# Kernel optimization log

Measured on AMD Instinct MI355X. Metric: run time of the kernel, lower is better.

The kernel has to match this reference:

```python
import jax, jax.numpy as jnp
import numpy as np
import math

D_MODEL = 512
N_HEADS = 8
D_K = D_MODEL // N_HEADS
N_SAMPLES = 16
BETA = 1.0
SCALE = 1.0 / math.sqrt(D_K)
PROPOSAL_TEMP = 0.5


def setup_inputs() -> dict:
    key = jax.random.key(0)
    ks = jax.random.split(key, 9)
    B, S = 2, 512
    x = jax.random.normal(ks[0], (B, S, D_MODEL), dtype=jnp.float32)
    init = lambda k: jax.random.normal(k, (D_MODEL, D_MODEL), dtype=jnp.float32) * 0.02
    return {
        "x": x,
        "Wq": init(ks[1]), "bq": jnp.zeros((D_MODEL,), jnp.float32),
        "Wk": init(ks[2]), "bk": jnp.zeros((D_MODEL,), jnp.float32),
        "Wv": init(ks[3]), "bv": jnp.zeros((D_MODEL,), jnp.float32),
        "Wo": init(ks[4]), "bo": jnp.zeros((D_MODEL,), jnp.float32),
    }


def _importance_sampled_weights(scores):
    # scores: [B,H,S,S]. Replicates the per-row Python loop, fully vectorized.
    B, H, Sq, Sk = scores.shape
    target = jax.nn.softmax(scores * BETA, axis=-1)            # [B,H,Sq,Sk]
    # optimal proposal: 0.5*target + 0.5*uniform
    prop = PROPOSAL_TEMP * target + (1.0 - PROPOSAL_TEMP) / Sk
    R = B * H * Sq
    tf = target.reshape(R, Sk)
    pf = prop.reshape(R, Sk)
    # tsu_backend.sample_binary_layer(log(p/(1-p))) == Bernoulli(p) sampling
    s = jax.random.bernoulli(jax.random.key(42), pf[:, None, :], (R, N_SAMPLES, Sk))
    # importance weight = prod(target[sel]) / (prod(prop[sel]) * prod(1-prop[~sel]))
    pt = jnp.prod(jnp.where(s, tf[:, None, :], 1.0), axis=-1)                 # [R,N]
    pp = jnp.prod(jnp.where(s, pf[:, None, :], 1.0 - pf[:, None, :]), axis=-1)
    valid = (s.sum(-1) > 0) & (pp > 0)
    w = jnp.where(valid, pt / jnp.maximum(pp, 1e-38), 0.0)
    ws = w.sum(-1, keepdims=True)
    w = jnp.where(ws > 0, w / jnp.maximum(ws, 1e-38), 1.0 / N_SAMPLES)        # [R,N]
    wa = jnp.einsum('rn,rnk->rk', w, s.astype(jnp.float32))                   # [R,Sk]
    was = wa.sum(-1, keepdims=True)
    wa = jnp.where(was > 0, wa / jnp.maximum(was, 1e-38), 1.0 / Sk)
    return wa.reshape(B, H, Sq, Sk)


def reference(x, Wq, bq, Wk, bk, Wv, bv, Wo, bo):
    B, S, Dm = x.shape
    proj = lambda W, b: (x @ W + b).reshape(B, S, N_HEADS, D_K).transpose(0, 2, 1, 3)
    Q = proj(Wq, bq)  # [B,H,S,dk]
    K = proj(Wk, bk)
    V = proj(Wv, bv)
    scores = jnp.einsum('bhqd,bhkd->bhqk', Q, K) * SCALE
    # torch builds weights via torch.tensor(...) which detaches => constant w.r.t. params
    attn = jax.lax.stop_gradient(_importance_sampled_weights(scores))
    out = jnp.einsum('bhqk,bhkd->bhqd', attn, V)
    out = out.transpose(0, 2, 1, 3).reshape(B, S, Dm)
    return out @ Wo + bo
```

## Files before the change

kernel.cpp:

```cpp
#include <hip/hip_runtime.h>
#include <cstdint>
#include <cstddef>


#define ROTL(x, r) __builtin_rotateleft32((x), (r))

#define QR8(s)                                                                \
  x0[0]+=x1[0];x0[1]+=x1[1];x0[2]+=x1[2];x0[3]+=x1[3];                        \
  x0[4]+=x1[4];x0[5]+=x1[5];x0[6]+=x1[6];x0[7]+=x1[7];                        \
  x1[0]=ROTL(x1[0],s);x1[1]=ROTL(x1[1],s);x1[2]=ROTL(x1[2],s);                \
  x1[3]=ROTL(x1[3],s);x1[4]=ROTL(x1[4],s);x1[5]=ROTL(x1[5],s);                \
  x1[6]=ROTL(x1[6],s);x1[7]=ROTL(x1[7],s);                                    \
  x1[0]^=x0[0];x1[1]^=x0[1];x1[2]^=x0[2];x1[3]^=x0[3];                        \
  x1[4]^=x0[4];x1[5]^=x0[5];x1[6]^=x0[6];x1[7]^=x0[7];
#define INJ8(X, Y)                                                            \
  x0[0]+=(X);x0[1]+=(X);x0[2]+=(X);x0[3]+=(X);                                \
  x0[4]+=(X);x0[5]+=(X);x0[6]+=(X);x0[7]+=(X);                                \
  x1[0]+=(Y);x1[1]+=(Y);x1[2]+=(Y);x1[3]+=(Y);                                \
  x1[4]+=(Y);x1[5]+=(Y);x1[6]+=(Y);x1[7]+=(Y);
#define INJ8Y(Y)                                                              \
  x1[0]+=(Y);x1[1]+=(Y);x1[2]+=(Y);x1[3]+=(Y);                                \
  x1[4]+=(Y);x1[5]+=(Y);x1[6]+=(Y);x1[7]+=(Y);

#define WAVE_FENCE() asm volatile("s_waitcnt lgkmcnt(0)" ::: "memory")

__global__ __launch_bounds__(256)
void qkv_gemm(const float* __restrict__ x,
              const float* __restrict__ Wq, const float* __restrict__ bq,
              const float* __restrict__ Wk, const float* __restrict__ bk,
              const float* __restrict__ Wv, const float* __restrict__ bv,
              const float* __restrict__ bo, float* __restrict__ outp,
              float* __restrict__ Qw, float* __restrict__ KTw,
              float* __restrict__ Vw) {
  const int tid = threadIdx.x;
  if (blockIdx.z == 3) {
    const int blk = blockIdx.y * 32 + blockIdx.x;
    const size_t base4 = (size_t)blk * 512 + tid;
    const float4* bo4 = (const float4*)bo;
    float4* out4 = (float4*)outp;
    out4[base4] = bo4[base4 & 127];
    out4[base4 + 256] = bo4[(base4 + 256) & 127];
    return;
  }
  const float* W; const float* bias;
  if (blockIdx.z == 0)      { W = Wq; bias = bq; }
  else if (blockIdx.z == 1) { W = Wk; bias = bk; }
  else                      { W = Wv; bias = bv; }

  __shared__ __align__(16) float smem[32 * 34 + 32 * 64];
  float (*At)[34] = (float(*)[34])smem;
  float (*Bs)[64] = (float(*)[64])(smem + 32 * 34);
  float (*T2)[34] = (float(*)[34])smem;

  const int tx = tid & 15, ty = tid >> 4;
  const int row0 = blockIdx.x * 32, col0 = blockIdx.y * 64;
  float acc[2][4] = {};

  const int ar = tid >> 3;
  const int kc = (tid & 7) << 2;
  const int br0 = tid >> 4,         bc0 = (tid & 15) << 2;
  const int br1 = (tid + 256) >> 4, bc1 = ((tid + 256) & 15) << 2;

  float4 aR, bR0, bR1;
  aR  = *(const float4*)&x[(size_t)(row0 + ar) * 512 + kc];
  bR0 = *(const float4*)&W[(size_t)br0 * 512 + col0 + bc0];
  bR1 = *(const float4*)&W[(size_t)br1 * 512 + col0 + bc1];

  for (int kk = 0; kk < 512; kk += 32) {
    At[kc + 0][ar] = aR.x; At[kc + 1][ar] = aR.y;
    At[kc + 2][ar] = aR.z; At[kc + 3][ar] = aR.w;
    *(float4*)&Bs[br0][bc0] = bR0;
    *(float4*)&Bs[br1][bc1] = bR1;
    __syncthreads();
    if (kk < 480) {
      const int kn = kk + 32;
      aR  = *(const float4*)&x[(size_t)(row0 + ar) * 512 + kn + kc];
      bR0 = *(const float4*)&W[(size_t)(kn + br0) * 512 + col0 + bc0];
      bR1 = *(const float4*)&W[(size_t)(kn + br1) * 512 + col0 + bc1];
    }
#pragma unroll
    for (int p = 0; p < 32; ++p) {
      const float2 a2 = *(const float2*)&At[p][ty << 1];
      const float4 b4 = *(const float4*)&Bs[p][tx << 2];
      acc[0][0] = fmaf(a2.x, b4.x, acc[0][0]); acc[0][1] = fmaf(a2.x, b4.y, acc[0][1]);
      acc[0][2] = fmaf(a2.x, b4.z, acc[0][2]); acc[0][3] = fmaf(a2.x, b4.w, acc[0][3]);
      acc[1][0] = fmaf(a2.y, b4.x, acc[1][0]); acc[1][1] = fmaf(a2.y, b4.y, acc[1][1]);
      acc[1][2] = fmaf(a2.y, b4.z, acc[1][2]); acc[1][3] = fmaf(a2.y, b4.w, acc[1][3]);
    }
    __syncthreads();
  }

  const int h = blockIdx.y;
  if (blockIdx.z == 0 || blockIdx.z == 2) {
    float* dst = (blockIdx.z == 0) ? Qw : Vw;
#pragma unroll
    for (int i = 0; i < 2; ++i) {
      const int row = row0 + (ty << 1) + i;
      const int b = row >> 9, s = row & 511;
#pragma unroll
      for (int j = 0; j < 4; ++j) {
        const int col = col0 + (tx << 2) + j;
        const int d = col & 63;
        dst[(((size_t)(b * 8 + h) * 512 + s) * 64) + d] = acc[i][j] + bias[col];
      }
    }
  } else {
#pragma unroll
    for (int i = 0; i < 2; ++i) {
#pragma unroll
      for (int j = 0; j < 4; ++j) {
        const int col = col0 + (tx << 2) + j;
        T2[(tx << 2) + j][(ty << 1) + i] = acc[i][j] + bias[col];
      }
    }
    __syncthreads();
    const int b = row0 >> 9;
    const int s0 = row0 & 511;
#pragma unroll
    for (int i2 = 0; i2 < 2; ++i2) {
      const int idx = tid + (i2 << 8);
      const int c = idx >> 3, seg = idx & 7;
      float* dst = KTw + (((size_t)(b * 8 + h) * 64 + c) << 9) + s0 + (seg << 2);
      *(float4*)dst = *(const float4*)&T2[c][seg << 2];
    }
  }
}

__global__ __launch_bounds__(256)
void fused_sample(const float* __restrict__ Q, const float* __restrict__ KT,
                  const float* __restrict__ V, const float* __restrict__ Wo,
                  float* __restrict__ outp) {
  const int tid = threadIdx.x;
  const int w = tid >> 6, l = tid & 63;
  const int blk = blockIdx.x;
  const int swz = ((blk & 7) << 8) | (blk >> 3);
  const int r = (swz << 2) + w;
  const int bh = r >> 9, q = r & 511;
  const int b = r >> 12, h = (r >> 9) & 7;

  __shared__ __align__(16) float    qs[4][64];
  __shared__ __align__(16) float    tfs[4][512];
  __shared__ __align__(16) uint32_t thru[4][512];

  float* tf = tfs[w];
  uint32_t* thr = thru[w];
  uint4* thr4 = (uint4*)thr;
  float* wa = (float*)thr;

  qs[w][l] = Q[((size_t)bh * 512 + q) * 64 + l];
  WAVE_FENCE();

  float s0 = 0.f, s1 = 0.f, s2 = 0.f, s3 = 0.f;
  float s4 = 0.f, s5 = 0.f, s6 = 0.f, s7 = 0.f;
  {
    const float* Kp = KT + (size_t)bh * 64 * 512 + (l << 2);
#pragma unroll 4
    for (int d4 = 0; d4 < 16; ++d4) {
      const float4 qv = *(const float4*)&qs[w][d4 << 2];
#pragma unroll
      for (int c = 0; c < 4; ++c) {
        const float qd = (c == 0) ? qv.x : (c == 1) ? qv.y : (c == 2) ? qv.z : qv.w;
        const size_t off = (size_t)(d4 * 4 + c) * 512;
        const float4 ka = *(const float4*)&Kp[off];
        const float4 kb = *(const float4*)&Kp[off + 256];
        s0 = fmaf(qd, ka.x, s0); s1 = fmaf(qd, ka.y, s1);
        s2 = fmaf(qd, ka.z, s2); s3 = fmaf(qd, ka.w, s3);
        s4 = fmaf(qd, kb.x, s4); s5 = fmaf(qd, kb.y, s5);
        s6 = fmaf(qd, kb.z, s6); s7 = fmaf(qd, kb.w, s7);
      }
    }
    s0 *= 0.125f; s1 *= 0.125f; s2 *= 0.125f; s3 *= 0.125f;
    s4 *= 0.125f; s5 *= 0.125f; s6 *= 0.125f; s7 *= 0.125f;
  }

  float mx = fmaxf(fmaxf(fmaxf(s0, s1), fmaxf(s2, s3)),
                   fmaxf(fmaxf(s4, s5), fmaxf(s6, s7)));
#pragma unroll
  for (int m = 1; m < 64; m <<= 1) mx = fmaxf(mx, __shfl_xor(mx, m));
  const float e0 = expf(s0 - mx), e1 = expf(s1 - mx);
  const float e2 = expf(s2 - mx), e3 = expf(s3 - mx);
  const float e4 = expf(s4 - mx), e5 = expf(s5 - mx);
  const float e6 = expf(s6 - mx), e7 = expf(s7 - mx);
  float tot = ((e0 + e1) + (e2 + e3)) + ((e4 + e5) + (e6 + e7));
#pragma unroll
  for (int m = 1; m < 64; m <<= 1) tot += __shfl_xor(tot, m);
  const float t0 = e0 / tot, t1 = e1 / tot, t2 = e2 / tot, t3 = e3 / tot;
  const float t4 = e4 / tot, t5 = e5 / tot, t6 = e6 / tot, t7 = e7 / tot;
  const float p0 = fmaf(0.5f, t0, 0.0009765625f);
  const float p1 = fmaf(0.5f, t1, 0.0009765625f);
  const float p2 = fmaf(0.5f, t2, 0.0009765625f);
  const float p3 = fmaf(0.5f, t3, 0.0009765625f);
  const float p4 = fmaf(0.5f, t4, 0.0009765625f);
  const float p5 = fmaf(0.5f, t5, 0.0009765625f);
  const float p6 = fmaf(0.5f, t6, 0.0009765625f);
  const float p7 = fmaf(0.5f, t7, 0.0009765625f);
  {
    *(float4*)&tf[l << 2]         = make_float4(t0, t1, t2, t3);
    *(float4*)&tf[256 + (l << 2)] = make_float4(t4, t5, t6, t7);
    uint4 ta, tb;
    ta.x = ((uint32_t)ceilf(p0 * 8388608.0f)) << 9;
    ta.y = ((uint32_t)ceilf(p1 * 8388608.0f)) << 9;
    ta.z = ((uint32_t)ceilf(p2 * 8388608.0f)) << 9;
    ta.w = ((uint32_t)ceilf(p3 * 8388608.0f)) << 9;
    tb.x = ((uint32_t)ceilf(p4 * 8388608.0f)) << 9;
    tb.y = ((uint32_t)ceilf(p5 * 8388608.0f)) << 9;
    tb.z = ((uint32_t)ceilf(p6 * 8388608.0f)) << 9;
    tb.w = ((uint32_t)ceilf(p7 * 8388608.0f)) << 9;
    thr4[((l & 31) << 2) + (l >> 5)]     = ta;
    thr4[((l & 31) << 2) + (l >> 5) + 2] = tb;
  }
  float ql = (((1.f - p0) * (1.f - p1)) * ((1.f - p2) * (1.f - p3))) *
             (((1.f - p4) * (1.f - p5)) * ((1.f - p6) * (1.f - p7)));
#pragma unroll
  for (int m = 1; m < 64; m <<= 1) ql *= __shfl_xor(ql, m);
  const float Qrow = ql;
  WAVE_FENCE();

  const int n = l >> 2, gl = l & 3;
  const uint32_t cbase =
      (uint32_t)r * 8192u + (uint32_t)n * 512u + (uint32_t)(gl << 7) + 42u;
  unsigned long long lo = 0ull, hi = 0ull;
  for (int u = 0; u < 16; ++u) {
    uint32_t x0[8], x1[8];
    const uint32_t cb = cbase + (uint32_t)(u << 3);
#pragma unroll
    for (int i = 0; i < 8; ++i) {
      const uint32_t c = cb + (uint32_t)i;
      x0[i] = c;
      x1[i] = ROTL(c, 13) ^ c;
    }
    QR8(15) QR8(26) QR8(6)
    INJ8(42u, 0x1BD11BF1u)
    QR8(17) QR8(29) QR8(16) QR8(24)
    INJ8(0x1BD11BF0u, 2u)
    QR8(13) QR8(15) QR8(26) QR8(6)
    INJ8Y(45u)
    QR8(17) QR8(29) QR8(16) QR8(24)
    INJ8(42u, 0x1BD11BF4u)
    QR8(13) QR8(15) QR8(26) QR8(6)
    INJ8(0x1BD11BF0u, 5u)
    const uint4 pA = thr4[(u << 3) + gl];
    const uint4 pB = thr4[(u << 3) + 4 + gl];
    uint32_t byte = 0u;
    byte |= (uint32_t)((x0[0] ^ x1[0]) < pA.x) << 0;
    byte |= (uint32_t)((x0[1] ^ x1[1]) < pA.y) << 1;
    byte |= (uint32_t)((x0[2] ^ x1[2]) < pA.z) << 2;
    byte |= (uint32_t)((x0[3] ^ x1[3]) < pA.w) << 3;
    byte |= (uint32_t)((x0[4] ^ x1[4]) < pB.x) << 4;
    byte |= (uint32_t)((x0[5] ^ x1[5]) < pB.y) << 5;
    byte |= (uint32_t)((x0[6] ^ x1[6]) < pB.z) << 6;
    byte |= (uint32_t)((x0[7] ^ x1[7]) < pB.w) << 7;
    const int sh = (u & 7) << 3;
    if (u < 8) lo |= (unsigned long long)byte << sh;
    else       hi |= (unsigned long long)byte << sh;
  }

  float ptl = 1.f, ratl = 1.f;
  int cl = __popcll(lo) + __popcll(hi);
  {
    unsigned long long bb = lo;
    while (bb) {
      const int j = __builtin_ctzll(bb);
      bb &= bb - 1ull;
      const float tv = tf[(gl << 7) + j];
      const float p = fmaf(0.5f, tv, 0.0009765625f);
      ptl *= tv;
      ratl *= p / (1.f - p);
    }
    bb = hi;
    while (bb) {
      const int j = __builtin_ctzll(bb);
      bb &= bb - 1ull;
      const float tv = tf[(gl << 7) + 64 + j];
      const float p = fmaf(0.5f, tv, 0.0009765625f);
      ptl *= tv;
      ratl *= p / (1.f - p);
    }
  }
#pragma unroll
  for (int m = 1; m < 4; m <<= 1) {
    ptl *= __shfl_xor(ptl, m);
    ratl *= __shfl_xor(ratl, m);
    cl += __shfl_xor(cl, m);
  }
  const float pp = Qrow * ratl;
  const float wl = (cl > 0 && pp > 0.f) ? (ptl / fmaxf(pp, 1e-38f)) : 0.f;
  float wsum = (gl == 0) ? wl : 0.f;
#pragma unroll
  for (int m = 1; m < 64; m <<= 1) wsum += __shfl_xor(wsum, m);
  const float wn = (wsum > 0.f) ? (wl / fmaxf(wsum, 1e-38f)) : 0.0625f;

  WAVE_FENCE();
  *(float4*)&wa[l << 2]         = make_float4(0.f, 0.f, 0.f, 0.f);
  *(float4*)&wa[256 + (l << 2)] = make_float4(0.f, 0.f, 0.f, 0.f);
  WAVE_FENCE();
  {
    unsigned long long bb = lo;
    while (bb) {
      const int j = __builtin_ctzll(bb);
      bb &= bb - 1ull;
      atomicAdd(&wa[(gl << 7) + j], wn);
    }
    bb = hi;
    while (bb) {
      const int j = __builtin_ctzll(bb);
      bb &= bb - 1ull;
      atomicAdd(&wa[(gl << 7) + 64 + j], wn);
    }
  }
  WAVE_FENCE();

  float sp = 0.f;
#pragma unroll
  for (int c = 0; c < 8; ++c) sp += wa[(c << 6) + l];
#pragma unroll
  for (int m = 1; m < 64; m <<= 1) sp += __shfl_xor(sp, m);
  const float was = sp;

  const float* Vb = V + ((size_t)(b * 8 + h) * 512) * 64;
  float o = 0.f;
  if (was > 0.f) {
    const float inv = 1.f / fmaxf(was, 1e-38f);
#pragma unroll 1
    for (int c = 0; c < 8; ++c) {
      const float v = wa[(c << 6) + l];
      unsigned long long mask = __ballot(v > 0.f);
      while (mask) {
        const int j = __builtin_ctzll(mask);
        mask &= mask - 1ull;
        const int k = (c << 6) + j;
        const float wv = wa[k];
        o = fmaf(wv * inv, Vb[(size_t)k * 64 + l], o);
      }
    }
  } else {
    for (int k = 0; k < 512; ++k) o += Vb[(size_t)k * 64 + l];
    o *= 0.001953125f;
  }

  {
    const float* Wh = Wo + ((size_t)h * 64) * 512 + l;
    float a0 = 0.f, a1 = 0.f, a2 = 0.f, a3 = 0.f;
    float a4 = 0.f, a5 = 0.f, a6 = 0.f, a7 = 0.f;
#pragma unroll 4
    for (int dd = 0; dd < 64; ++dd) {
      const float ov = __shfl(o, dd);
      const float* wrow = Wh + (size_t)dd * 512;
      a0 = fmaf(ov, wrow[0],   a0);
      a1 = fmaf(ov, wrow[64],  a1);
      a2 = fmaf(ov, wrow[128], a2);
      a3 = fmaf(ov, wrow[192], a3);
      a4 = fmaf(ov, wrow[256], a4);
      a5 = fmaf(ov, wrow[320], a5);
      a6 = fmaf(ov, wrow[384], a6);
      a7 = fmaf(ov, wrow[448], a7);
    }
    float* orow = outp + ((size_t)(b * 512 + q)) * 512 + l;
    atomicAdd(&orow[0],   a0);
    atomicAdd(&orow[64],  a1);
    atomicAdd(&orow[128], a2);
    atomicAdd(&orow[192], a3);
    atomicAdd(&orow[256], a4);
    atomicAdd(&orow[320], a5);
    atomicAdd(&orow[384], a6);
    atomicAdd(&orow[448], a7);
  }
}

extern "C" void kernel_launch(void* const* d_in, const int* in_sizes, int n_in,
                              void* d_out, int out_size, void* d_ws,
                              size_t ws_size, hipStream_t stream) {
  const float* x  = (const float*)d_in[0];
  const float* Wq = (const float*)d_in[1];
  const float* bq = (const float*)d_in[2];
  const float* Wk = (const float*)d_in[3];
  const float* bk = (const float*)d_in[4];
  const float* Wv = (const float*)d_in[5];
  const float* bv = (const float*)d_in[6];
  const float* Wo = (const float*)d_in[7];
  const float* bo = (const float*)d_in[8];
  float* out = (float*)d_out;

  float* ws = (float*)d_ws;
  float* Qw = ws;
  float* KT = ws + 524288;
  float* Vw = ws + 1048576;

  dim3 gq(32, 8, 4);
  qkv_gemm<<<gq, 256, 0, stream>>>(x, Wq, bq, Wk, bk, Wv, bv, bo, out,
                                   Qw, KT, Vw);
  fused_sample<<<2048, 256, 0, stream>>>(Qw, KT, Vw, Wo, out);
}
```

Baseline: 283.4 us.

## Share K and Wo loads across the block's four query rows and double-buffer the projection GEMM

The projection GEMM now double-buffers its shared-memory tiles, so each k-step needs one barrier instead of two and the next tile's stores follow the compute. In the sampling kernel, the QK^T scores are computed cooperatively: each thread reads K once and produces scores for all four query rows of the block, instead of each wave reading K separately. The Wo output projection likewise loads each Wo element once per block for four rows, using a shared transposed buffer of the head outputs. This cuts global and L2 traffic for K and Wo by about four times, at the cost of extra block-wide barriers and more shared memory.

Result: faster. 274.9 us (-3.0%).

```diff
diff --git a/kernel.cpp b/kernel.cpp
--- a/kernel.cpp
+++ b/kernel.cpp
@@ -47,10 +47,12 @@
   else if (blockIdx.z == 1) { W = Wk; bias = bk; }
   else                      { W = Wv; bias = bv; }
 
-  __shared__ __align__(16) float smem[32 * 34 + 32 * 64];
-  float (*At)[34] = (float(*)[34])smem;
-  float (*Bs)[64] = (float(*)[64])(smem + 32 * 34);
-  float (*T2)[34] = (float(*)[34])smem;
+  __shared__ __align__(16) float smem[2 * (32 * 34 + 32 * 64)];
+  float (*At0)[34] = (float(*)[34])smem;
+  float (*Bs0)[64] = (float(*)[64])(smem + 32 * 34);
+  float (*At1)[34] = (float(*)[34])(smem + 3136);
+  float (*Bs1)[64] = (float(*)[64])(smem + 3136 + 32 * 34);
+  float (*T2)[34]  = (float(*)[34])smem;
 
   const int tx = tid & 15, ty = tid >> 4;
   const int row0 = blockIdx.x * 32, col0 = blockIdx.y * 64;
@@ -66,12 +68,16 @@
   bR0 = *(const float4*)&W[(size_t)br0 * 512 + col0 + bc0];
   bR1 = *(const float4*)&W[(size_t)br1 * 512 + col0 + bc1];
 
+  At0[kc + 0][ar] = aR.x; At0[kc + 1][ar] = aR.y;
+  At0[kc + 2][ar] = aR.z; At0[kc + 3][ar] = aR.w;
+  *(float4*)&Bs0[br0][bc0] = bR0;
+  *(float4*)&Bs0[br1][bc1] = bR1;
+  __syncthreads();
+
+  float (*Atc)[34] = At0; float (*Bsc)[64] = Bs0;
+  float (*Atn)[34] = At1; float (*Bsn)[64] = Bs1;
+
   for (int kk = 0; kk < 512; kk += 32) {
-    At[kc + 0][ar] = aR.x; At[kc + 1][ar] = aR.y;
-    At[kc + 2][ar] = aR.z; At[kc + 3][ar] = aR.w;
-    *(float4*)&Bs[br0][bc0] = bR0;
-    *(float4*)&Bs[br1][bc1] = bR1;
-    __syncthreads();
     if (kk < 480) {
       const int kn = kk + 32;
       aR  = *(const float4*)&x[(size_t)(row0 + ar) * 512 + kn + kc];
@@ -80,14 +86,22 @@
     }
 #pragma unroll
     for (int p = 0; p < 32; ++p) {
-      const float2 a2 = *(const float2*)&At[p][ty << 1];
-      const float4 b4 = *(const float4*)&Bs[p][tx << 2];
+      const float2 a2 = *(const float2*)&Atc[p][ty << 1];
+      const float4 b4 = *(const float4*)&Bsc[p][tx << 2];
       acc[0][0] = fmaf(a2.x, b4.x, acc[0][0]); acc[0][1] = fmaf(a2.x, b4.y, acc[0][1]);
       acc[0][2] = fmaf(a2.x, b4.z, acc[0][2]); acc[0][3] = fmaf(a2.x, b4.w, acc[0][3]);
       acc[1][0] = fmaf(a2.y, b4.x, acc[1][0]); acc[1][1] = fmaf(a2.y, b4.y, acc[1][1]);
       acc[1][2] = fmaf(a2.y, b4.z, acc[1][2]); acc[1][3] = fmaf(a2.y, b4.w, acc[1][3]);
     }
+    if (kk < 480) {
+      Atn[kc + 0][ar] = aR.x; Atn[kc + 1][ar] = aR.y;
+      Atn[kc + 2][ar] = aR.z; Atn[kc + 3][ar] = aR.w;
+      *(float4*)&Bsn[br0][bc0] = bR0;
+      *(float4*)&Bsn[br1][bc1] = bR1;
+    }
     __syncthreads();
+    float (*tA)[34] = Atc; Atc = Atn; Atn = tA;
+    float (*tB)[64] = Bsc; Bsc = Bsn; Bsn = tB;
   }
 
   const int h = blockIdx.y;
@@ -130,57 +144,77 @@
 void fused_sample(const float* __restrict__ Q, const float* __restrict__ KT,
                   const float* __restrict__ V, const float* __restrict__ Wo,
                   float* __restrict__ outp) {
+  const int bx = blockIdx.x;
+  const int rbase = ((((bx & 7) << 8) | (bx >> 3)) << 2);
+  const int bh = rbase >> 9, q0 = rbase & 511;
+  const int b = rbase >> 12, h = (rbase >> 9) & 7;
   const int tid = threadIdx.x;
   const int w = tid >> 6, l = tid & 63;
-  const int blk = blockIdx.x;
-  const int swz = ((blk & 7) << 8) | (blk >> 3);
-  const int r = (swz << 2) + w;
-  const int bh = r >> 9, q = r & 511;
-  const int b = r >> 12, h = (r >> 9) & 7;
 
   __shared__ __align__(16) float    qs[4][64];
-  __shared__ __align__(16) float    tfs[4][512];
-  __shared__ __align__(16) uint32_t thru[4][512];
-
-  float* tf = tfs[w];
-  uint32_t* thr = thru[w];
+  __shared__ __align__(16) float    scs[4][512];
+  __shared__ __align__(16) uint32_t pscu[4][512];
+  __shared__ __align__(16) float    o_sT[64][4];
+
+  qs[w][l] = Q[((size_t)bh * 512 + q0 + w) * 64 + l];
+  __syncthreads();
+
+  {
+    const float* Kp = KT + (size_t)bh * 64 * 512 + tid;
+    float s00 = 0.f, s01 = 0.f, s10 = 0.f, s11 = 0.f;
+    float s20 = 0.f, s21 = 0.f, s30 = 0.f, s31 = 0.f;
+#pragma unroll
+    for (int d4 = 0; d4 < 16; ++d4) {
+      float k0v[4], k1v[4];
+#pragma unroll
+      for (int j = 0; j < 4; ++j) {
+        k0v[j] = Kp[(size_t)(d4 * 4 + j) * 512];
+        k1v[j] = Kp[(size_t)(d4 * 4 + j) * 512 + 256];
+      }
+      const float4 q0v = *(const float4*)&qs[0][d4 << 2];
+      const float4 q1v = *(const float4*)&qs[1][d4 << 2];
+      const float4 q2v = *(const float4*)&qs[2][d4 << 2];
+      const float4 q3v = *(const float4*)&qs[3][d4 << 2];
+      s00 = fmaf(q0v.x, k0v[0], s00); s00 = fmaf(q0v.y, k0v[1], s00);
+      s00 = fmaf(q0v.z, k0v[2], s00); s00 = fmaf(q0v.w, k0v[3], s00);
+      s01 = fmaf(q0v.x, k1v[0], s01); s01 = fmaf(q0v.y, k1v[1], s01);
+      s01 = fmaf(q0v.z, k1v[2], s01); s01 = fmaf(q0v.w, k1v[3], s01);
+      s10 = fmaf(q1v.x, k0v[0], s10); s10 = fmaf(q1v.y, k0v[1], s10);
+      s10 = fmaf(q1v.z, k0v[2], s10); s10 = fmaf(q1v.w, k0v[3], s10);
+      s11 = fmaf(q1v.x, k1v[0], s11); s11 = fmaf(q1v.y, k1v[1], s11);
+      s11 = fmaf(q1v.z, k1v[2], s11); s11 = fmaf(q1v.w, k1v[3], s11);
+      s20 = fmaf(q2v.x, k0v[0], s20); s20 = fmaf(q2v.y, k0v[1], s20);
+      s20 = fmaf(q2v.z, k0v[2], s20); s20 = fmaf(q2v.w, k0v[3], s20);
+      s21 = fmaf(q2v.x, k1v[0], s21); s21 = fmaf(q2v.y, k1v[1], s21);
+      s21 = fmaf(q2v.z, k1v[2], s21); s21 = fmaf(q2v.w, k1v[3], s21);
+      s30 = fmaf(q3v.x, k0v[0], s30); s30 = fmaf(q3v.y, k0v[1], s30);
+      s30 = fmaf(q3v.z, k0v[2], s30); s30 = fmaf(q3v.w, k0v[3], s30);
+      s31 = fmaf(q3v.x, k1v[0], s31); s31 = fmaf(q3v.y, k1v[1], s31);
+      s31 = fmaf(q3v.z, k1v[2], s31); s31 = fmaf(q3v.w, k1v[3], s31);
+    }
+    scs[0][tid] = s00 * 0.125f; scs[0][tid + 256] = s01 * 0.125f;
+    scs[1][tid] = s10 * 0.125f; scs[1][tid + 256] = s11 * 0.125f;
+    scs[2][tid] = s20 * 0.125f; scs[2][tid + 256] = s21 * 0.125f;
+    scs[3][tid] = s30 * 0.125f; scs[3][tid + 256] = s31 * 0.125f;
+  }
+  __syncthreads();
+
+  const int r = rbase + w;
+  float* tf = scs[w];
+  uint32_t* thr = pscu[w];
   uint4* thr4 = (uint4*)thr;
   float* wa = (float*)thr;
 
-  qs[w][l] = Q[((size_t)bh * 512 + q) * 64 + l];
-  WAVE_FENCE();
-
-  float s0 = 0.f, s1 = 0.f, s2 = 0.f, s3 = 0.f;
-  float s4 = 0.f, s5 = 0.f, s6 = 0.f, s7 = 0.f;
-  {
-    const float* Kp = KT + (size_t)bh * 64 * 512 + (l << 2);
-#pragma unroll 4
-    for (int d4 = 0; d4 < 16; ++d4) {
-      const float4 qv = *(const float4*)&qs[w][d4 << 2];
-#pragma unroll
-      for (int c = 0; c < 4; ++c) {
-        const float qd = (c == 0) ? qv.x : (c == 1) ? qv.y : (c == 2) ? qv.z : qv.w;
-        const size_t off = (size_t)(d4 * 4 + c) * 512;
-        const float4 ka = *(const float4*)&Kp[off];
-        const float4 kb = *(const float4*)&Kp[off + 256];
-        s0 = fmaf(qd, ka.x, s0); s1 = fmaf(qd, ka.y, s1);
-        s2 = fmaf(qd, ka.z, s2); s3 = fmaf(qd, ka.w, s3);
-        s4 = fmaf(qd, kb.x, s4); s5 = fmaf(qd, kb.y, s5);
-        s6 = fmaf(qd, kb.z, s6); s7 = fmaf(qd, kb.w, s7);
-      }
-    }
-    s0 *= 0.125f; s1 *= 0.125f; s2 *= 0.125f; s3 *= 0.125f;
-    s4 *= 0.125f; s5 *= 0.125f; s6 *= 0.125f; s7 *= 0.125f;
-  }
-
-  float mx = fmaxf(fmaxf(fmaxf(s0, s1), fmaxf(s2, s3)),
-                   fmaxf(fmaxf(s4, s5), fmaxf(s6, s7)));
+  const float4 sa = *(const float4*)&tf[l << 2];
+  const float4 sb = *(const float4*)&tf[256 + (l << 2)];
+  float mx = fmaxf(fmaxf(fmaxf(sa.x, sa.y), fmaxf(sa.z, sa.w)),
+                   fmaxf(fmaxf(sb.x, sb.y), fmaxf(sb.z, sb.w)));
 #pragma unroll
   for (int m = 1; m < 64; m <<= 1) mx = fmaxf(mx, __shfl_xor(mx, m));
-  const float e0 = expf(s0 - mx), e1 = expf(s1 - mx);
-  const float e2 = expf(s2 - mx), e3 = expf(s3 - mx);
-  const float e4 = expf(s4 - mx), e5 = expf(s5 - mx);
-  const float e6 = expf(s6 - mx), e7 = expf(s7 - mx);
+  const float e0 = expf(sa.x - mx), e1 = expf(sa.y - mx);
+  const float e2 = expf(sa.z - mx), e3 = expf(sa.w - mx);
+  const float e4 = expf(sb.x - mx), e5 = expf(sb.y - mx);
+  const float e6 = expf(sb.z - mx), e7 = expf(sb.w - mx);
   float tot = ((e0 + e1) + (e2 + e3)) + ((e4 + e5) + (e6 + e7));
 #pragma unroll
   for (int m = 1; m < 64; m <<= 1) tot += __shfl_xor(tot, m);
@@ -337,33 +371,28 @@
     for (int k = 0; k < 512; ++k) o += Vb[(size_t)k * 64 + l];
     o *= 0.001953125f;
   }
+  o_sT[l][w] = o;
+  __syncthreads();
 
   {
-    const float* Wh = Wo + ((size_t)h * 64) * 512 + l;
-    float a0 = 0.f, a1 = 0.f, a2 = 0.f, a3 = 0.f;
-    float a4 = 0.f, a5 = 0.f, a6 = 0.f, a7 = 0.f;
-#pragma unroll 4
+    const float* Wh = Wo + ((size_t)h * 64) * 512;
+    float a00 = 0.f, a01 = 0.f, a10 = 0.f, a11 = 0.f;
+    float a20 = 0.f, a21 = 0.f, a30 = 0.f, a31 = 0.f;
+#pragma unroll 8
     for (int dd = 0; dd < 64; ++dd) {
-      const float ov = __shfl(o, dd);
-      const float* wrow = Wh + (size_t)dd * 512;
-      a0 = fmaf(ov, wrow[0],   a0);
-      a1 = fmaf(ov, wrow[64],  a1);
-      a2 = fmaf(ov, wrow[128], a2);
-      a3 = fmaf(ov, wrow[192], a3);
-      a4 = fmaf(ov, wrow[256], a4);
-      a5 = fmaf(ov, wrow[320], a5);
-      a6 = fmaf(ov, wrow[384], a6);
-      a7 = fmaf(ov, wrow[448], a7);
-    }
-    float* orow = outp + ((size_t)(b * 512 + q)) * 512 + l;
-    atomicAdd(&orow[0],   a0);
-    atomicAdd(&orow[64],  a1);
-    atomicAdd(&orow[128], a2);
-    atomicAdd(&orow[192], a3);
-    atomicAdd(&orow[256], a4);
-    atomicAdd(&orow[320], a5);
-    atomicAdd(&orow[384], a6);
-    atomicAdd(&orow[448], a7);
+      const float4 o4 = *(const float4*)&o_sT[dd][0];
+      const float w0 = Wh[(size_t)dd * 512 + tid];
+      const float w1 = Wh[(size_t)dd * 512 + tid + 256];
+      a00 = fmaf(o4.x, w0, a00); a01 = fmaf(o4.x, w1, a01);
+      a10 = fmaf(o4.y, w0, a10); a11 = fmaf(o4.y, w1, a11);
+      a20 = fmaf(o4.z, w0, a20); a21 = fmaf(o4.z, w1, a21);
+      a30 = fmaf(o4.w, w0, a30); a31 = fmaf(o4.w, w1, a31);
+    }
+    float* orow = outp + ((size_t)(b * 512 + q0)) * 512;
+    atomicAdd(&orow[tid], a00);         atomicAdd(&orow[tid + 256], a01);
+    atomicAdd(&orow[512 + tid], a10);   atomicAdd(&orow[512 + tid + 256], a11);
+    atomicAdd(&orow[1024 + tid], a20);  atomicAdd(&orow[1024 + tid + 256], a21);
+    atomicAdd(&orow[1536 + tid], a30);  atomicAdd(&orow[1536 + tid + 256], a31);
   }
 }
 
```
